# Kernel tuning notes

Hardware: AMD Instinct MI355X
Metric: run time of the kernel (lower is better)

Reference implementation:

```python
import jax, jax.numpy as jnp
import numpy as np

NEG_INF = float('-inf')


def setup_inputs() -> dict:
    key = jax.random.key(0)
    ks = jax.random.split(key, 5)
    B, S, D = 2, 4096, 2048
    H, Hd, R = 16, 64, 64  # heads, head_dim, dq_rank
    ratio = 4
    sc = 0.02
    return {
        'hidden': jax.random.normal(ks[0], (B, S, D), jnp.float32),
        'w_dq': jax.random.normal(ks[1], (D, R), jnp.float32) * sc,
        'w_iuq': jax.random.normal(ks[2], (R, H * Hd), jnp.float32) * sc,
        'w_w': jax.random.normal(ks[3], (D, H), jnp.float32) * sc,
        'w_comp': jax.random.normal(ks[4], (ratio * D, Hd), jnp.float32) * sc,
        'compress_ratio': ratio,
        'index_topk': 256,
    }


def reference(hidden, w_dq, w_iuq, w_w, w_comp, compress_ratio, index_topk):
    B, S, D = hidden.shape
    r = int(compress_ratio)
    K = int(index_topk)
    P = S // r
    H = w_w.shape[1]
    Hd = w_iuq.shape[1] // H

    # mini-Compressor: linear over concatenated windows of r tokens -> [B,P,Hd]
    k_icomp = hidden.reshape(B, P, r * D) @ w_comp

    # low-rank query projection: [B,S,R] -> [B,S,H,Hd]
    q_i = ((hidden @ w_dq) @ w_iuq).reshape(B, S, H, Hd)
    w_i = hidden @ w_w  # [B,S,H]

    relu = jax.nn.relu(jnp.einsum('bshd,bpd->bshp', q_i, k_icomp))
    scores = jnp.einsum('bshp,bsh->bsp', relu, w_i)  # weighted head-sum

    # causal mask over compressed pool: pool s covers [s*r,(s+1)*r); allowed iff window end <= t
    t_idx = jnp.arange(S)[:, None]
    s_end = (jnp.arange(P)[None, :] + 1) * r - 1
    mask = jnp.where(s_end <= t_idx, 0.0, NEG_INF).astype(scores.dtype)
    scores = scores + mask[None]

    k_eff = min(K, P)
    topk_scores, topk_idxs = jax.lax.top_k(scores, k_eff)
    topk_idxs = jnp.where(jnp.isneginf(topk_scores), -1, topk_idxs)
    if k_eff < K:
        pad_i = jnp.full((B, S, K - k_eff), -1, topk_idxs.dtype)
        pad_s = jnp.full((B, S, K - k_eff), NEG_INF, topk_scores.dtype)
        topk_idxs = jnp.concatenate([topk_idxs, pad_i], axis=-1)
        topk_scores = jnp.concatenate([topk_scores, pad_s], axis=-1)
    return topk_idxs, topk_scores
```

## Files before the change

kernel.cpp:

```cpp
#include <hip/hip_runtime.h>

constexpr int S_    = 4096;
constexpr int D_    = 2048;
constexpr int H_    = 16;
constexpr int HD_   = 64;
constexpr int P_    = 1024;
constexpr int TOPK_ = 256;
constexpr int ROWS_ = 8192;

#define NEGINF (-__builtin_inff())
#define MASK_SENTINEL (-3.0e38f)

typedef __attribute__((ext_vector_type(8))) short bf16x8;
typedef __attribute__((ext_vector_type(4))) float f32x4;
typedef unsigned long long u64;

static __device__ __forceinline__ unsigned short f32_to_bf16_rne(float x) {
  unsigned u = __float_as_uint(x);
  u += 0x7FFFu + ((u >> 16) & 1u);
  return (unsigned short)(u >> 16);
}
static __device__ __forceinline__ float bf16_to_f32(unsigned short h) {
  return __uint_as_float(((unsigned)h) << 16);
}

static __device__ __forceinline__ void split8(const float4 a, const float4 b,
                                              bf16x8& hi, bf16x8& lo) {
  const float x[8] = {a.x, a.y, a.z, a.w, b.x, b.y, b.z, b.w};
#pragma unroll
  for (int i = 0; i < 8; ++i) {
    const unsigned u = __float_as_uint(x[i]);
    const float r = x[i] - __uint_as_float(u & 0xFFFF0000u);
    hi[i] = (short)(u >> 16);
    lo[i] = (short)(__float_as_uint(r) >> 16);
  }
}

__global__ void conv_w(const float* __restrict__ wdq, const float* __restrict__ ww,
                       const float* __restrict__ wc,
                       unsigned short* __restrict__ bdh, unsigned short* __restrict__ bdl,
                       unsigned short* __restrict__ bwh, unsigned short* __restrict__ bwl,
                       unsigned short* __restrict__ bch, unsigned short* __restrict__ bcl) {
  const int i = blockIdx.x * 256 + threadIdx.x;
  float x;
  unsigned short *oh, *ol;
  int oi;
  if (i < 131072) {
    const int n = i >> 11, k = i & 2047;
    x = wdq[(size_t)k * 64 + n]; oh = bdh; ol = bdl; oi = i;
  } else if (i < 163840) {
    const int j = i - 131072;
    const int n = j >> 11, k = j & 2047;
    x = ww[(size_t)k * 16 + n]; oh = bwh; ol = bwl; oi = j;
  } else {
    const int j = i - 163840;
    if (j >= 524288) return;
    const int n = j >> 13, k = j & 8191;
    x = wc[(size_t)k * 64 + n]; oh = bch; ol = bcl; oi = j;
  }
  const unsigned u = __float_as_uint(x);
  const float r = x - __uint_as_float(u & 0xFFFF0000u);
  oh[oi] = (unsigned short)(u >> 16);
  ol[oi] = (unsigned short)(__float_as_uint(r) >> 16);
}

__global__ __launch_bounds__(256) void mfma_a(
    const float* __restrict__ hid,
    const unsigned short* __restrict__ bdh, const unsigned short* __restrict__ bdl,
    const unsigned short* __restrict__ bwh, const unsigned short* __restrict__ bwl,
    float* __restrict__ part1,
    float* __restrict__ part3) {
  const int t = threadIdx.x;
  const int w = t >> 6, lane = t & 63;
  const int m = lane & 15, quad = lane >> 4;
  const int m0 = blockIdx.x << 6;
  const int z  = blockIdx.y;
  const int r0 = m0 + (w << 4);
  const int kb = z << 8;

  f32x4 acc[5];
#pragma unroll
  for (int i = 0; i < 5; ++i) acc[i] = f32x4{0.f, 0.f, 0.f, 0.f};

  const float* ap = hid + (size_t)(r0 + m) * D_ + kb + (quad << 3);

#pragma unroll 1
  for (int ks = 0; ks < 8; ++ks) {
    const int koff = ks << 5;
    const float4 a0 = *(const float4*)(ap + koff);
    const float4 a1 = *(const float4*)(ap + koff + 4);
    bf16x8 Ah, Al;
    split8(a0, a1, Ah, Al);
    const size_t kcol = (size_t)(kb + koff + (quad << 3));
#pragma unroll
    for (int nt = 0; nt < 4; ++nt) {
      const size_t bo = (size_t)((nt << 4) + m) * D_ + kcol;
      const bf16x8 Bh = *(const bf16x8*)(bdh + bo);
      const bf16x8 Bl = *(const bf16x8*)(bdl + bo);
      f32x4 c = acc[nt];
      c = __builtin_amdgcn_mfma_f32_16x16x32_bf16(Ah, Bh, c, 0, 0, 0);
      c = __builtin_amdgcn_mfma_f32_16x16x32_bf16(Al, Bh, c, 0, 0, 0);
      c = __builtin_amdgcn_mfma_f32_16x16x32_bf16(Ah, Bl, c, 0, 0, 0);
      acc[nt] = c;
    }
    {
      const size_t bo = (size_t)m * D_ + kcol;
      const bf16x8 Bh = *(const bf16x8*)(bwh + bo);
      const bf16x8 Bl = *(const bf16x8*)(bwl + bo);
      f32x4 c = acc[4];
      c = __builtin_amdgcn_mfma_f32_16x16x32_bf16(Ah, Bh, c, 0, 0, 0);
      c = __builtin_amdgcn_mfma_f32_16x16x32_bf16(Al, Bh, c, 0, 0, 0);
      c = __builtin_amdgcn_mfma_f32_16x16x32_bf16(Ah, Bl, c, 0, 0, 0);
      acc[4] = c;
    }
  }

  float* p1 = part1 + (size_t)z * (ROWS_ * 64);
#pragma unroll
  for (int nt = 0; nt < 4; ++nt)
#pragma unroll
    for (int i = 0; i < 4; ++i)
      p1[(size_t)(r0 + (quad << 2) + i) * 64 + (nt << 4) + m] = acc[nt][i];
  float* p3 = part3 + (size_t)z * (ROWS_ * H_);
#pragma unroll
  for (int i = 0; i < 4; ++i)
    p3[(size_t)(r0 + (quad << 2) + i) * H_ + m] = acc[4][i];
}

__global__ __launch_bounds__(256) void mfma_g4(
    const float* __restrict__ hid,
    const unsigned short* __restrict__ bch, const unsigned short* __restrict__ bcl,
    float* __restrict__ part4) {
  const int t = threadIdx.x;
  const int w = t >> 6, lane = t & 63;
  const int m = lane & 15, quad = lane >> 4;
  const int m0 = blockIdx.x << 6;
  const int z  = blockIdx.y;
  const int r0 = m0 + (w << 4);
  const int kb = z << 9;

  f32x4 acc[4];
#pragma unroll
  for (int i = 0; i < 4; ++i) acc[i] = f32x4{0.f, 0.f, 0.f, 0.f};

  const float* ap = hid + (size_t)(r0 + m) * 8192 + kb + (quad << 3);

#pragma unroll 1
  for (int ks = 0; ks < 16; ++ks) {
    const int koff = ks << 5;
    const float4 a0 = *(const float4*)(ap + koff);
    const float4 a1 = *(const float4*)(ap + koff + 4);
    bf16x8 Ah, Al;
    split8(a0, a1, Ah, Al);
    const size_t kcol = (size_t)(kb + koff + (quad << 3));
#pragma unroll
    for (int nt = 0; nt < 4; ++nt) {
      const size_t bo = (size_t)((nt << 4) + m) * 8192 + kcol;
      const bf16x8 Bh = *(const bf16x8*)(bch + bo);
      const bf16x8 Bl = *(const bf16x8*)(bcl + bo);
      f32x4 c = acc[nt];
      c = __builtin_amdgcn_mfma_f32_16x16x32_bf16(Ah, Bh, c, 0, 0, 0);
      c = __builtin_amdgcn_mfma_f32_16x16x32_bf16(Al, Bh, c, 0, 0, 0);
      c = __builtin_amdgcn_mfma_f32_16x16x32_bf16(Ah, Bl, c, 0, 0, 0);
      acc[nt] = c;
    }
  }

  float* p4 = part4 + (size_t)z * (2048 * 64);
#pragma unroll
  for (int nt = 0; nt < 4; ++nt)
#pragma unroll
    for (int i = 0; i < 4; ++i)
      p4[(size_t)(r0 + (quad << 2) + i) * 64 + (nt << 4) + m] = acc[nt][i];
}

__global__ __launch_bounds__(256) void gemm64_bs(const float* __restrict__ A,
                                                 const float* __restrict__ B,
                                                 unsigned short* __restrict__ Ch,
                                                 unsigned short* __restrict__ Cl,
                                                 int M, int N, int K) {
  const int t  = threadIdx.x;
  const int tx = t & 15, ty = t >> 4;
  const int n0 = blockIdx.x << 6;
  const int m0 = blockIdx.y << 6;

  __shared__ float As[16][68];
  __shared__ float Bs[16][64];
  float acc[4][4] = {};

  const int am = t >> 2, ak = (t & 3) << 2;
  const int bk = t >> 4, bn = (t & 15) << 2;
  const float* Ap = A + (size_t)(m0 + am) * K + ak;
  const float* Bp = B + (size_t)bk * N + n0 + bn;

  for (int kk = 0; kk < K; kk += 16) {
    const float4 a4 = *(const float4*)(Ap + kk);
    const float4 b4 = *(const float4*)(Bp + (size_t)kk * N);
    __syncthreads();
    As[ak + 0][am] = a4.x; As[ak + 1][am] = a4.y;
    As[ak + 2][am] = a4.z; As[ak + 3][am] = a4.w;
    *(float4*)&Bs[bk][bn] = b4;
    __syncthreads();
#pragma unroll
    for (int k = 0; k < 16; ++k) {
      const float4 av = *(const float4*)&As[k][ty << 2];
      const float4 bv = *(const float4*)&Bs[k][tx << 2];
      acc[0][0] += av.x * bv.x; acc[0][1] += av.x * bv.y; acc[0][2] += av.x * bv.z; acc[0][3] += av.x * bv.w;
      acc[1][0] += av.y * bv.x; acc[1][1] += av.y * bv.y; acc[1][2] += av.y * bv.z; acc[1][3] += av.y * bv.w;
      acc[2][0] += av.z * bv.x; acc[2][1] += av.z * bv.y; acc[2][2] += av.z * bv.z; acc[2][3] += av.z * bv.w;
      acc[3][0] += av.w * bv.x; acc[3][1] += av.w * bv.y; acc[3][2] += av.w * bv.z; acc[3][3] += av.w * bv.w;
    }
  }
#pragma unroll
  for (int i = 0; i < 4; ++i) {
    const size_t off = (size_t)(m0 + (ty << 2) + i) * N + n0 + (tx << 2);
    ushort4 hv, lv;
    float v;
    v = acc[i][0]; hv.x = f32_to_bf16_rne(v); lv.x = f32_to_bf16_rne(v - bf16_to_f32(hv.x));
    v = acc[i][1]; hv.y = f32_to_bf16_rne(v); lv.y = f32_to_bf16_rne(v - bf16_to_f32(hv.y));
    v = acc[i][2]; hv.z = f32_to_bf16_rne(v); lv.z = f32_to_bf16_rne(v - bf16_to_f32(hv.z));
    v = acc[i][3]; hv.w = f32_to_bf16_rne(v); lv.w = f32_to_bf16_rne(v - bf16_to_f32(hv.w));
    *(ushort4*)&Ch[off] = hv;
    *(ushort4*)&Cl[off] = lv;
  }
}

__global__ void reduce_sum(const float* __restrict__ part, float* __restrict__ out,
                           int n, int Z) {
  const int i = blockIdx.x * blockDim.x + threadIdx.x;
  if (i >= n) return;
  float s = part[i];
  for (int z = 1; z < Z; ++z) s += part[(size_t)z * n + i];
  out[i] = s;
}

__global__ void reduce_k_split(const float* __restrict__ part,
                               unsigned short* __restrict__ kh,
                               unsigned short* __restrict__ kl) {
  const int i = blockIdx.x * blockDim.x + threadIdx.x;
  if (i >= 2048 * HD_) return;
  const int n = 2048 * HD_;
  float s = 0.f;
#pragma unroll
  for (int z = 0; z < 16; ++z) s += part[(size_t)z * n + i];
  const unsigned short h = f32_to_bf16_rne(s);
  kh[i] = h;
  kl[i] = f32_to_bf16_rne(s - bf16_to_f32(h));
}

__global__ __launch_bounds__(256, 4) void score_mfma(
    const unsigned short* __restrict__ qh,
    const unsigned short* __restrict__ ql,
    const float* __restrict__ wi,
    const unsigned short* __restrict__ kh,
    const unsigned short* __restrict__ kl,
    float* __restrict__ scores_out) {
  __shared__ float wis[16][16];

  const int t    = threadIdx.x;
  const int w    = t >> 6;
  const int lane = t & 63;
  const int m    = lane & 15;
  const int quad = lane >> 4;
  const int bid  = blockIdx.x;
  const int g    = (bid & 7) | ((bid >> 5) << 3);
  const int qq   = (bid >> 3) & 3;
  const int row0 = g << 4;
  const int b    = row0 >> 12;
  const int p0   = (qq << 8) + (w << 6);

  if (t < 64)
    *(float4*)&wis[t >> 2][(t & 3) << 2] =
        *(const float4*)(wi + (size_t)(row0 + (t >> 2)) * H_ + ((t & 3) << 2));
  __syncthreads();

  const size_t kbase = ((size_t)(b << 10) + p0 + m) * 64 + (quad << 3);
  bf16x8 Bh[4][2], Bl[4][2];
#pragma unroll
  for (int nt = 0; nt < 4; ++nt) {
    const size_t ko = kbase + (size_t)(nt << 4) * 64;
    Bh[nt][0] = *(const bf16x8*)(kh + ko);
    Bh[nt][1] = *(const bf16x8*)(kh + ko + 32);
    Bl[nt][0] = *(const bf16x8*)(kl + ko);
    Bl[nt][1] = *(const bf16x8*)(kl + ko + 32);
  }

  float acc[4][4];
#pragma unroll
  for (int nt = 0; nt < 4; ++nt)
#pragma unroll
    for (int r = 0; r < 4; ++r) acc[nt][r] = 0.f;

  const size_t qbase = (size_t)(row0 + m) * 1024 + (quad << 3);

#pragma unroll 1
  for (int h = 0; h < 16; ++h) {
    const size_t qo = qbase + (size_t)h * 64;
    const bf16x8 Ah0 = *(const bf16x8*)(qh + qo);
    const bf16x8 Ah1 = *(const bf16x8*)(qh + qo + 32);
    const bf16x8 Al0 = *(const bf16x8*)(ql + qo);
    const bf16x8 Al1 = *(const bf16x8*)(ql + qo + 32);
    float wreg[4];
#pragma unroll
    for (int r = 0; r < 4; ++r) wreg[r] = wis[(quad << 2) + r][h];
#pragma unroll
    for (int nt = 0; nt < 4; ++nt) {
      f32x4 c = {0.f, 0.f, 0.f, 0.f};
      c = __builtin_amdgcn_mfma_f32_16x16x32_bf16(Ah0, Bh[nt][0], c, 0, 0, 0);
      c = __builtin_amdgcn_mfma_f32_16x16x32_bf16(Ah1, Bh[nt][1], c, 0, 0, 0);
      c = __builtin_amdgcn_mfma_f32_16x16x32_bf16(Al0, Bh[nt][0], c, 0, 0, 0);
      c = __builtin_amdgcn_mfma_f32_16x16x32_bf16(Al1, Bh[nt][1], c, 0, 0, 0);
      c = __builtin_amdgcn_mfma_f32_16x16x32_bf16(Ah0, Bl[nt][0], c, 0, 0, 0);
      c = __builtin_amdgcn_mfma_f32_16x16x32_bf16(Ah1, Bl[nt][1], c, 0, 0, 0);
#pragma unroll
      for (int r = 0; r < 4; ++r)
        acc[nt][r] += wreg[r] * fmaxf(c[r], 0.f);
    }
  }

  float* so = scores_out + (size_t)(row0 + (quad << 2)) * 1024 + p0 + m;
#pragma unroll
  for (int r = 0; r < 4; ++r)
#pragma unroll
    for (int nt = 0; nt < 4; ++nt)
      so[(size_t)r * 1024 + (nt << 4)] = acc[nt][r];
}

template <int K2, int J2>
static __device__ __forceinline__ void substage(u64* E, int lane) {
  if constexpr (J2 >= 16) {
    constexpr int XM = J2 >> 4;
    const bool lower = (lane & XM) == 0;
#pragma unroll
    for (int v = 0; v < 16; ++v) {
      const int e = (lane << 4) | v;
      const u64 p = __shfl_xor(E[v], XM, 64);
      const bool up = (e & K2) == 0;
      const bool keepmin = (up == lower);
      const u64 mn = (E[v] < p) ? E[v] : p;
      const u64 mx = (E[v] < p) ? p : E[v];
      E[v] = keepmin ? mn : mx;
    }
  } else {
#pragma unroll
    for (int v = 0; v < 16; ++v) {
      if ((v & J2) == 0) {
        const int e = (lane << 4) | v;
        const bool up = (e & K2) == 0;
        const u64 a = E[v], b = E[v | J2];
        const u64 mn = (a < b) ? a : b;
        const u64 mx = (a < b) ? b : a;
        E[v]      = up ? mn : mx;
        E[v | J2] = up ? mx : mn;
      }
    }
  }
}

template <int K2, int J2>
static __device__ __forceinline__ void substages(u64* E, int lane) {
  substage<K2, J2>(E, lane);
  if constexpr (J2 > 1) substages<K2, (J2 >> 1)>(E, lane);
}

static __device__ __forceinline__ void sort1024(u64* E, int lane) {
  substages<2, 1>(E, lane);
  substages<4, 2>(E, lane);
  substages<8, 4>(E, lane);
  substages<16, 8>(E, lane);
  substages<32, 16>(E, lane);
  substages<64, 32>(E, lane);
  substages<128, 64>(E, lane);
  substages<256, 128>(E, lane);
  substages<512, 256>(E, lane);
  substages<1024, 512>(E, lane);
}

__global__ __launch_bounds__(256) void topk_sort(
    const float* __restrict__ scores,
    float* __restrict__ out_idx, float* __restrict__ out_sc) {
  const int t    = threadIdx.x;
  const int w    = t >> 6;
  const int lane = t & 63;
  const int row  = (blockIdx.x << 2) + w;
  const int s    = row & (S_ - 1);
  const int plim = (s + 1) >> 2;

  const float* sr = scores + (size_t)row * 1024 + (lane << 4);
  u64 E[16];
#pragma unroll
  for (int v4 = 0; v4 < 4; ++v4) {
    const float4 f = *(const float4*)(sr + (v4 << 2));
    const float sv[4] = {f.x, f.y, f.z, f.w};
#pragma unroll
    for (int j = 0; j < 4; ++j) {
      const int v = (v4 << 2) + j;
      const int e = (lane << 4) | v;
      const float sc = (e < plim) ? sv[j] : NEGINF;
      const unsigned u  = __float_as_uint(sc);
      const unsigned mm = (u & 0x80000000u) ? ~u : (u | 0x80000000u);
      E[v] = ((u64)(mm ^ 0xFFFFFFFFu) << 32) | (unsigned)e;
    }
  }
  sort1024(E, lane);
  if (lane < 16) {
    const size_t ob = (size_t)row * TOPK_ + (lane << 4);
#pragma unroll
    for (int v4 = 0; v4 < 4; ++v4) {
      float vi[4], vs[4];
#pragma unroll
      for (int j = 0; j < 4; ++j) {
        const u64 kk = E[(v4 << 2) + j];
        const unsigned idx = (unsigned)kk;
        const unsigned mm  = (unsigned)(kk >> 32) ^ 0xFFFFFFFFu;
        const unsigned u   = (mm & 0x80000000u) ? (mm ^ 0x80000000u) : ~mm;
        const float sc = __uint_as_float(u);
        const bool masked = (sc == NEGINF);
        vi[j] = masked ? -1.0f : (float)idx;
        vs[j] = masked ? MASK_SENTINEL : sc;
      }
      *(float4*)&out_idx[ob + (v4 << 2)] = make_float4(vi[0], vi[1], vi[2], vi[3]);
      *(float4*)&out_sc[ob + (v4 << 2)]  = make_float4(vs[0], vs[1], vs[2], vs[3]);
    }
  }
}

extern "C" void kernel_launch(void* const* d_in, const int* in_sizes, int n_in,
                              void* d_out, int out_size, void* d_ws, size_t ws_size,
                              hipStream_t stream) {
  const float* hidden = (const float*)d_in[0];
  const float* w_dq   = (const float*)d_in[1];
  const float* w_iuq  = (const float*)d_in[2];
  const float* w_w    = (const float*)d_in[3];
  const float* w_comp = (const float*)d_in[4];

  float* ws = (float*)d_ws;
  float* tmp_dq = ws;
  float* w_i    = tmp_dq + 524288;
  unsigned short* qh = (unsigned short*)(w_i + 131072);
  unsigned short* ql = qh + 8388608;
  unsigned short* kh = ql + 8388608;
  unsigned short* kl = kh + 131072;
  float* scores = (float*)(kl + 131072);
  unsigned short* bdh = (unsigned short*)(scores + 8388608);
  unsigned short* bdl = bdh + 131072;
  unsigned short* bwh = bdl + 131072;
  unsigned short* bwl = bwh + 32768;
  unsigned short* bch = bwl + 32768;
  unsigned short* bcl = bch + 524288;
  float* part1 = scores;
  float* part3 = part1 + 8 * 524288;
  float* part4 = part3 + 8 * 131072;

  conv_w<<<dim3(2688), 256, 0, stream>>>(w_dq, w_w, w_comp,
                                         bdh, bdl, bwh, bwl, bch, bcl);
  mfma_a<<<dim3(128, 8), 256, 0, stream>>>(hidden, bdh, bdl, bwh, bwl, part1, part3);
  reduce_sum<<<dim3(524288 / 256), 256, 0, stream>>>(part1, tmp_dq, 524288, 8);
  reduce_sum<<<dim3(131072 / 256), 256, 0, stream>>>(part3, w_i, 131072, 8);
  mfma_g4<<<dim3(32, 16), 256, 0, stream>>>(hidden, bch, bcl, part4);
  reduce_k_split<<<dim3(131072 / 256), 256, 0, stream>>>(part4, kh, kl);
  gemm64_bs<<<dim3(16, 128, 1), 256, 0, stream>>>(tmp_dq, w_iuq, qh, ql, ROWS_, 1024, 64);
  score_mfma<<<dim3(ROWS_ / 16 * 4), 256, 0, stream>>>(qh, ql, w_i, kh, kl, scores);
  float* out_idx = (float*)d_out;
  float* out_sc  = out_idx + (size_t)ROWS_ * TOPK_;
  topk_sort<<<dim3(ROWS_ / 4), 256, 0, stream>>>(scores, out_idx, out_sc);
}
```

Baseline: 376.4 us.

## Split top-k sort by causal prefix length into smaller bitonic sorts

Replaces the single 1024-element bitonic sort per row with three kernels chosen by sequence position. Rows in the first quarter have at most 256 valid pool entries, so they run a 256-element sort with four rows per wavefront. Rows in the second quarter run a 512-element sort with two rows per wavefront, and the rest keep the full sort. This removes sorting work on masked entries, at the cost of two extra kernel launches.

```diff
diff --git a/kernel.cpp b/kernel.cpp
--- a/kernel.cpp
+++ b/kernel.cpp
@@ -326,14 +326,14 @@
       so[(size_t)r * 1024 + (nt << 4)] = acc[nt][r];
 }
 
-template <int K2, int J2>
+template <int K2, int J2, int LM>
 static __device__ __forceinline__ void substage(u64* E, int lane) {
   if constexpr (J2 >= 16) {
     constexpr int XM = J2 >> 4;
     const bool lower = (lane & XM) == 0;
 #pragma unroll
     for (int v = 0; v < 16; ++v) {
-      const int e = (lane << 4) | v;
+      const int e = ((lane & LM) << 4) | v;
       const u64 p = __shfl_xor(E[v], XM, 64);
       const bool up = (e & K2) == 0;
       const bool keepmin = (up == lower);
@@ -345,7 +345,7 @@
 #pragma unroll
     for (int v = 0; v < 16; ++v) {
       if ((v & J2) == 0) {
-        const int e = (lane << 4) | v;
+        const int e = ((lane & LM) << 4) | v;
         const bool up = (e & K2) == 0;
         const u64 a = E[v], b = E[v | J2];
         const u64 mn = (a < b) ? a : b;
@@ -357,37 +357,14 @@
   }
 }
 
-template <int K2, int J2>
+template <int K2, int J2, int LM>
 static __device__ __forceinline__ void substages(u64* E, int lane) {
-  substage<K2, J2>(E, lane);
-  if constexpr (J2 > 1) substages<K2, (J2 >> 1)>(E, lane);
-}
-
-static __device__ __forceinline__ void sort1024(u64* E, int lane) {
-  substages<2, 1>(E, lane);
-  substages<4, 2>(E, lane);
-  substages<8, 4>(E, lane);
-  substages<16, 8>(E, lane);
-  substages<32, 16>(E, lane);
-  substages<64, 32>(E, lane);
-  substages<128, 64>(E, lane);
-  substages<256, 128>(E, lane);
-  substages<512, 256>(E, lane);
-  substages<1024, 512>(E, lane);
-}
-
-__global__ __launch_bounds__(256) void topk_sort(
-    const float* __restrict__ scores,
-    float* __restrict__ out_idx, float* __restrict__ out_sc) {
-  const int t    = threadIdx.x;
-  const int w    = t >> 6;
-  const int lane = t & 63;
-  const int row  = (blockIdx.x << 2) + w;
-  const int s    = row & (S_ - 1);
-  const int plim = (s + 1) >> 2;
-
-  const float* sr = scores + (size_t)row * 1024 + (lane << 4);
-  u64 E[16];
+  substage<K2, J2, LM>(E, lane);
+  if constexpr (J2 > 1) substages<K2, (J2 >> 1), LM>(E, lane);
+}
+
+static __device__ __forceinline__ void load_enc(const float* __restrict__ sr,
+                                                int ebase, int plim, u64* E) {
 #pragma unroll
   for (int v4 = 0; v4 < 4; ++v4) {
     const float4 f = *(const float4*)(sr + (v4 << 2));
@@ -395,33 +372,120 @@
 #pragma unroll
     for (int j = 0; j < 4; ++j) {
       const int v = (v4 << 2) + j;
-      const int e = (lane << 4) | v;
+      const int e = ebase + v;
       const float sc = (e < plim) ? sv[j] : NEGINF;
       const unsigned u  = __float_as_uint(sc);
       const unsigned mm = (u & 0x80000000u) ? ~u : (u | 0x80000000u);
       E[v] = ((u64)(mm ^ 0xFFFFFFFFu) << 32) | (unsigned)e;
     }
   }
-  sort1024(E, lane);
+}
+
+static __device__ __forceinline__ void dec_write(const u64* E, float* __restrict__ oi,
+                                                 float* __restrict__ os) {
+#pragma unroll
+  for (int v4 = 0; v4 < 4; ++v4) {
+    float vi[4], vs[4];
+#pragma unroll
+    for (int j = 0; j < 4; ++j) {
+      const u64 kk = E[(v4 << 2) + j];
+      const unsigned idx = (unsigned)kk;
+      const unsigned mm  = (unsigned)(kk >> 32) ^ 0xFFFFFFFFu;
+      const unsigned u   = (mm & 0x80000000u) ? (mm ^ 0x80000000u) : ~mm;
+      const float sc = __uint_as_float(u);
+      const bool masked = (sc == NEGINF);
+      vi[j] = masked ? -1.0f : (float)idx;
+      vs[j] = masked ? MASK_SENTINEL : sc;
+    }
+    *(float4*)&oi[v4 << 2] = make_float4(vi[0], vi[1], vi[2], vi[3]);
+    *(float4*)&os[v4 << 2] = make_float4(vs[0], vs[1], vs[2], vs[3]);
+  }
+}
+
+
+__global__ __launch_bounds__(256) void topk_q0(
+    const float* __restrict__ scores, float* __restrict__ out_idx,
+    float* __restrict__ out_sc) {
+  const int t    = threadIdx.x;
+  const int w    = t >> 6;
+  const int lane = t & 63;
+  const int g    = lane >> 4;
+  const int l16  = lane & 15;
+  const int j    = ((int)blockIdx.x << 4) + (w << 2) + g;
+  const int b    = j >> 10;
+  const int s    = j & 1023;
+  const int row  = (b << 12) + s;
+  const int plim = (s + 1) >> 2;
+  u64 E[16];
+  load_enc(scores + (size_t)row * 1024 + (l16 << 4), l16 << 4, plim, E);
+  substages<2, 1, 15>(E, lane);
+  substages<4, 2, 15>(E, lane);
+  substages<8, 4, 15>(E, lane);
+  substages<16, 8, 15>(E, lane);
+  substages<32, 16, 15>(E, lane);
+  substages<64, 32, 15>(E, lane);
+  substages<128, 64, 15>(E, lane);
+  substages<256, 128, 15>(E, lane);
+  const size_t ob = (size_t)row * TOPK_ + (l16 << 4);
+  dec_write(E, out_idx + ob, out_sc + ob);
+}
+
+__global__ __launch_bounds__(256) void topk_q1(
+    const float* __restrict__ scores, float* __restrict__ out_idx,
+    float* __restrict__ out_sc) {
+  const int t    = threadIdx.x;
+  const int w    = t >> 6;
+  const int lane = t & 63;
+  const int g    = lane >> 5;
+  const int l32  = lane & 31;
+  const int j    = ((int)blockIdx.x << 3) + (w << 1) + g;
+  const int b    = j >> 10;
+  const int s    = 1024 + (j & 1023);
+  const int row  = (b << 12) + s;
+  const int plim = (s + 1) >> 2;
+  u64 E[16];
+  load_enc(scores + (size_t)row * 1024 + (l32 << 4), l32 << 4, plim, E);
+  substages<2, 1, 31>(E, lane);
+  substages<4, 2, 31>(E, lane);
+  substages<8, 4, 31>(E, lane);
+  substages<16, 8, 31>(E, lane);
+  substages<32, 16, 31>(E, lane);
+  substages<64, 32, 31>(E, lane);
+  substages<128, 64, 31>(E, lane);
+  substages<256, 128, 31>(E, lane);
+  substages<512, 256, 31>(E, lane);
+  if (l32 < 16) {
+    const size_t ob = (size_t)row * TOPK_ + (l32 << 4);
+    dec_write(E, out_idx + ob, out_sc + ob);
+  }
+}
+
+__global__ __launch_bounds__(256) void topk_q23(
+    const float* __restrict__ scores, float* __restrict__ out_idx,
+    float* __restrict__ out_sc) {
+  const int t    = threadIdx.x;
+  const int w    = t >> 6;
+  const int lane = t & 63;
+  const int j    = ((int)blockIdx.x << 2) + w;
+  const int b    = j >> 11;
+  const int s    = 2048 + (j & 2047);
+  const int row  = (b << 12) + s;
+  const int plim = (s + 1) >> 2;
+  u64 E[16];
+  load_enc(scores + (size_t)row * 1024 + (lane << 4), lane << 4, plim, E);
+  substages<2, 1, 63>(E, lane);
+  substages<4, 2, 63>(E, lane);
+  substages<8, 4, 63>(E, lane);
+  substages<16, 8, 63>(E, lane);
+  substages<32, 16, 63>(E, lane);
+  substages<64, 32, 63>(E, lane);
+  substages<128, 64, 63>(E, lane);
+  substages<256, 128, 63>(E, lane);
+  substages<512, 256, 63>(E, lane);
+  substages<1024, 512, 63>(E, lane);
   if (lane < 16) {
     const size_t ob = (size_t)row * TOPK_ + (lane << 4);
-#pragma unroll
-    for (int v4 = 0; v4 < 4; ++v4) {
-      float vi[4], vs[4];
-#pragma unroll
-      for (int j = 0; j < 4; ++j) {
-        const u64 kk = E[(v4 << 2) + j];
-        const unsigned idx = (unsigned)kk;
-        const unsigned mm  = (unsigned)(kk >> 32) ^ 0xFFFFFFFFu;
-        const unsigned u   = (mm & 0x80000000u) ? (mm ^ 0x80000000u) : ~mm;
-        const float sc = __uint_as_float(u);
-        const bool masked = (sc == NEGINF);
-        vi[j] = masked ? -1.0f : (float)idx;
-        vs[j] = masked ? MASK_SENTINEL : sc;
-      }
-      *(float4*)&out_idx[ob + (v4 << 2)] = make_float4(vi[0], vi[1], vi[2], vi[3]);
-      *(float4*)&out_sc[ob + (v4 << 2)]  = make_float4(vs[0], vs[1], vs[2], vs[3]);
-    }
+    dec_write(E, out_idx + ob, out_sc + ob);
   }
 }
 
@@ -463,5 +527,7 @@
   score_mfma<<<dim3(ROWS_ / 16 * 4), 256, 0, stream>>>(qh, ql, w_i, kh, kl, scores);
   float* out_idx = (float*)d_out;
   float* out_sc  = out_idx + (size_t)ROWS_ * TOPK_;
-  topk_sort<<<dim3(ROWS_ / 4), 256, 0, stream>>>(scores, out_idx, out_sc);
-}
+  topk_q0<<<dim3(128), 256, 0, stream>>>(scores, out_idx, out_sc);
+  topk_q1<<<dim3(256), 256, 0, stream>>>(scores, out_idx, out_sc);
+  topk_q23<<<dim3(1024), 256, 0, stream>>>(scores, out_idx, out_sc);
+}
```

New measurement: 373.2 us. About the same (-0.8%).
